# Kernel optimization log

Measured on AMD Instinct MI355X. Metric: run time of the kernel, lower is better.

Reference implementation:

```python
import jax, jax.numpy as jnp
import numpy as np

TOPK = 12
D = 256
SCALE = D ** -0.5


def setup_inputs() -> dict:
    key = jax.random.key(0)
    ks = jax.random.split(key, 6)
    N, D_in = 12288, 1024
    def w(k, shape, fan_in):
        return jax.random.normal(k, shape, jnp.float32) / np.float32(np.sqrt(fan_in))
    return {
        "x_path": jax.random.normal(ks[0], (N, D_in), jnp.float32),
        "wsi_w": w(ks[1], (D_in, D), D_in),
        "wsi_b": jnp.zeros((D,), jnp.float32),
        "wh_w": w(ks[2], (D, D), D),
        "wh_b": jnp.zeros((D,), jnp.float32),
        "wt_w": w(ks[3], (D, D), D),
        "wt_b": jnp.zeros((D,), jnp.float32),
        "w1_w": w(ks[4], (D, D), D),
        "w1_b": jnp.zeros((D,), jnp.float32),
        "w2_w": w(ks[5], (D, D), D),
        "w2_b": jnp.zeros((D,), jnp.float32),
    }


def reference(x_path, wsi_w, wsi_b, wh_w, wh_b, wt_w, wt_b, w1_w, w1_b, w2_w, w2_b):
    # wsi_net: Linear(1024,256) + ReLU (dropout is identity in eval)
    h = jax.nn.relu(x_path @ wsi_w + wsi_b)          # [N, D]
    e_h = h @ wh_w + wh_b                            # [N, D]
    e_t = h @ wt_w + wt_b                            # [N, D]
    # dense scaled similarity: [N, N]
    attn_logit = (e_h * SCALE) @ e_t.T
    topk_weight, topk_index = jax.lax.top_k(attn_logit, TOPK)  # [N, K]
    topk_prob = jax.nn.softmax(topk_weight, axis=-1)           # [N, K]
    # gather top-k neighbor tail embeddings
    Nb_h = e_t[topk_index]                           # [N, K, D]
    # eh_r = p * Nb_h + (1-p) (x) e_h   (outer product == broadcast mul)
    eh_r = topk_prob[..., None] * Nb_h + (1.0 - topk_prob)[..., None] * e_h[:, None, :]
    gate = jnp.tanh(e_h[:, None, :] + eh_r)          # [N, K, D]
    ka_weight = jnp.einsum('nkd,nkd->nk', Nb_h, gate)  # [N, K]
    ka_prob = jax.nn.softmax(ka_weight, axis=-1)       # [N, K]
    e_Nh = jnp.einsum('nk,nkd->nd', ka_prob, Nb_h)     # [N, D]
    sum_embedding = jax.nn.relu((e_h + e_Nh) @ w1_w + w1_b)
    bi_embedding = jax.nn.relu((e_h * e_Nh) @ w2_w + w2_b)
    return sum_embedding + bi_embedding              # [N, D]
```

## Files before the change

kernel.cpp:

```cpp
#include <hip/hip_runtime.h>
#include <hip/hip_bf16.h>
#include <cmath>

#define TK 12
#define NROW 12288
#define NEG_BIG (-3.0e38f)
#define MFMA16(a,b,c) __builtin_amdgcn_mfma_f32_16x16x32_f16(a,b,c,0,0,0)

#define NCH 8
#define CTILES 96
#define NPH 48
#define NGRP_TOT 384
#define CAP 256

typedef _Float16 f16x8 __attribute__((ext_vector_type(8)));
typedef _Float16 f16x4 __attribute__((ext_vector_type(4)));
typedef float    f32x4 __attribute__((ext_vector_type(4)));

typedef __attribute__((address_space(1))) const void gvoid_t;
typedef __attribute__((address_space(3))) void lvoid_t;
__device__ __forceinline__ void gload_lds16(const void* g, void* l) {
    __builtin_amdgcn_global_load_lds((gvoid_t*)g, (lvoid_t*)l, 16, 0, 0);
}

__global__ __launch_bounds__(256) void wpack(
    const float* __restrict__ W, _Float16* __restrict__ hi,
    _Float16* __restrict__ lo, int N, int nkt)
{
    const int tid = blockIdx.x * 256 + threadIdx.x;
    const int l = tid & 63;
    const int s = (tid >> 6) % nkt;
    const int cg = tid / (nkt * 64);
    const int krow = s * 32 + 8 * (l >> 4);
    const int col = cg * 16 + (l & 15);
    f16x8 H, L;
    #pragma unroll
    for (int j = 0; j < 8; ++j) {
        float w = W[(size_t)(krow + j) * N + col];
        _Float16 h = (_Float16)w;
        H[j] = h;
        L[j] = (_Float16)(w - (float)h);
    }
    *(f16x8*)(hi + (size_t)tid * 8) = H;
    *(f16x8*)(lo + (size_t)tid * 8) = L;
}

__global__ __launch_bounds__(256) void wpack4(
    const float* __restrict__ W0, const float* __restrict__ W1,
    const float* __restrict__ W2, const float* __restrict__ W3,
    _Float16* __restrict__ base)
{
    const int m = blockIdx.y;
    const float* W = (m == 0) ? W0 : (m == 1) ? W1 : (m == 2) ? W2 : W3;
    _Float16* hi = base + (size_t)m * 131072;
    _Float16* lo = hi + 65536;
    const int tid = blockIdx.x * 256 + threadIdx.x;
    const int l = tid & 63;
    const int s = (tid >> 6) & 7;
    const int cg = tid >> 9;
    const int krow = s * 32 + 8 * (l >> 4);
    const int col = cg * 16 + (l & 15);
    f16x8 H, L;
    #pragma unroll
    for (int j = 0; j < 8; ++j) {
        float w = W[(size_t)(krow + j) * 256 + col];
        _Float16 h = (_Float16)w;
        H[j] = h;
        L[j] = (_Float16)(w - (float)h);
    }
    *(f16x8*)(hi + (size_t)tid * 8) = H;
    *(f16x8*)(lo + (size_t)tid * 8) = L;
}

template<bool RELU>
__global__ __launch_bounds__(256) void gemm_mfma(
    const float* __restrict__ A1,
    const _Float16* __restrict__ Wh, const _Float16* __restrict__ Wl,
    const float* __restrict__ bias, float* __restrict__ C, int K)
{
    __shared__ _Float16 aH[2048], aL[2048];
    __shared__ _Float16 wH[2048], wL[2048];
    const int tid = threadIdx.x, lane = tid & 63, wave = tid >> 6;
    const int rb = blockIdx.y * 64;
    const int cbg = blockIdx.x * 4;
    const int nkt = K >> 5;

    const int arow = rb + wave * 16 + (lane & 15);
    const int acol0 = 8 * (lane >> 4);
    const float* a1p = A1 + (size_t)arow * K + acol0;
    const size_t wbase = ((size_t)(cbg + wave) * nkt) * 512 + lane * 8;

    f32x4 acc[4];
    #pragma unroll
    for (int rg = 0; rg < 4; ++rg) acc[rg] = (f32x4){0.f,0.f,0.f,0.f};

    float4 pa0 = *(const float4*)(a1p);
    float4 pa1 = *(const float4*)(a1p + 4);
    f16x8 pwh = *(const f16x8*)(Wh + wbase);
    f16x8 pwl = *(const f16x8*)(Wl + wbase);

    for (int kt = 0; kt < nkt; ++kt) {
        __syncthreads();
        {
            float v[8] = {pa0.x, pa0.y, pa0.z, pa0.w, pa1.x, pa1.y, pa1.z, pa1.w};
            f16x8 H, L;
            #pragma unroll
            for (int j = 0; j < 8; ++j) {
                _Float16 h = (_Float16)v[j];
                H[j] = h;
                L[j] = (_Float16)(v[j] - (float)h);
            }
            *(f16x8*)&aH[tid*8] = H;
            *(f16x8*)&aL[tid*8] = L;
            *(f16x8*)&wH[tid*8] = pwh;
            *(f16x8*)&wL[tid*8] = pwl;
        }
        __syncthreads();
        if (kt + 1 < nkt) {
            pa0 = *(const float4*)(a1p + (kt+1)*32);
            pa1 = *(const float4*)(a1p + (kt+1)*32 + 4);
            pwh = *(const f16x8*)(Wh + wbase + (size_t)(kt+1)*512);
            pwl = *(const f16x8*)(Wl + wbase + (size_t)(kt+1)*512);
        }
        f16x8 wh = *(const f16x8*)&wH[(wave*64 + lane)*8];
        f16x8 wl = *(const f16x8*)&wL[(wave*64 + lane)*8];
        #pragma unroll
        for (int rg = 0; rg < 4; ++rg) {
            f16x8 ah = *(const f16x8*)&aH[(rg*64 + lane)*8];
            f16x8 al = *(const f16x8*)&aL[(rg*64 + lane)*8];
            acc[rg] = MFMA16(wh, ah, acc[rg]);
            acc[rg] = MFMA16(wl, ah, acc[rg]);
            acc[rg] = MFMA16(wh, al, acc[rg]);
        }
    }
    const int col = (cbg + wave)*16 + 4*(lane >> 4);
    float4 b4 = *(const float4*)(bias + col);
    #pragma unroll
    for (int rg = 0; rg < 4; ++rg) {
        const int row = rb + rg*16 + (lane & 15);
        float4 o;
        o.x = acc[rg][0] + b4.x; o.y = acc[rg][1] + b4.y;
        o.z = acc[rg][2] + b4.z; o.w = acc[rg][3] + b4.w;
        if (RELU) {
            o.x = fmaxf(o.x, 0.f); o.y = fmaxf(o.y, 0.f);
            o.z = fmaxf(o.z, 0.f); o.w = fmaxf(o.w, 0.f);
        }
        *(float4*)(C + (size_t)row*256 + col) = o;
    }
}

template<int DMODE>
__global__ __launch_bounds__(256) void gemm_dual(
    const float* __restrict__ A1, const float* __restrict__ A2,
    const _Float16* __restrict__ W1h, const _Float16* __restrict__ W1l,
    const _Float16* __restrict__ W2h, const _Float16* __restrict__ W2l,
    const float* __restrict__ bias1, const float* __restrict__ bias2,
    float* __restrict__ C1, float* __restrict__ C2,
    _Float16* __restrict__ P1, _Float16* __restrict__ P2)
{
    __shared__ _Float16 aH[2][2048], aL[2][2048];
    __shared__ _Float16 wH[2][2048], wL[2][2048];
    const int tid = threadIdx.x, lane = tid & 63, wave = tid >> 6;
    const int rb = blockIdx.y * 64;
    const int cbg = blockIdx.x * 4;

    const int arow = rb + wave * 16 + (lane & 15);
    const int acol0 = 8 * (lane >> 4);
    const float* a1p = A1 + (size_t)arow * 256 + acol0;
    const float* a2p = (DMODE == 1) ? (A2 + (size_t)arow * 256 + acol0) : nullptr;
    const size_t wbase = ((size_t)(cbg + wave) * 8) * 512 + lane * 8;

    f32x4 acc1[4], acc2[4];
    #pragma unroll
    for (int rg = 0; rg < 4; ++rg) {
        acc1[rg] = (f32x4){0.f,0.f,0.f,0.f};
        acc2[rg] = (f32x4){0.f,0.f,0.f,0.f};
    }

    float4 pa0 = *(const float4*)(a1p);
    float4 pa1 = *(const float4*)(a1p + 4);
    float4 pb0, pb1;
    if (DMODE == 1) { pb0 = *(const float4*)(a2p); pb1 = *(const float4*)(a2p + 4); }
    f16x8 pw1h = *(const f16x8*)(W1h + wbase);
    f16x8 pw1l = *(const f16x8*)(W1l + wbase);
    f16x8 pw2h = *(const f16x8*)(W2h + wbase);
    f16x8 pw2l = *(const f16x8*)(W2l + wbase);

    for (int kt = 0; kt < 8; ++kt) {
        __syncthreads();
        {
            float v[8] = {pa0.x, pa0.y, pa0.z, pa0.w, pa1.x, pa1.y, pa1.z, pa1.w};
            if (DMODE == 0) {
                f16x8 H, L;
                #pragma unroll
                for (int j = 0; j < 8; ++j) {
                    _Float16 h = (_Float16)v[j];
                    H[j] = h;
                    L[j] = (_Float16)(v[j] - (float)h);
                }
                *(f16x8*)&aH[0][tid*8] = H;
                *(f16x8*)&aL[0][tid*8] = L;
            } else {
                float b[8] = {pb0.x, pb0.y, pb0.z, pb0.w, pb1.x, pb1.y, pb1.z, pb1.w};
                f16x8 Hs, Ls, Hm, Lm;
                #pragma unroll
                for (int j = 0; j < 8; ++j) {
                    float s = v[j] + b[j];
                    float m = v[j] * b[j];
                    _Float16 hs = (_Float16)s;
                    _Float16 hm = (_Float16)m;
                    Hs[j] = hs; Ls[j] = (_Float16)(s - (float)hs);
                    Hm[j] = hm; Lm[j] = (_Float16)(m - (float)hm);
                }
                *(f16x8*)&aH[0][tid*8] = Hs;
                *(f16x8*)&aL[0][tid*8] = Ls;
                *(f16x8*)&aH[1][tid*8] = Hm;
                *(f16x8*)&aL[1][tid*8] = Lm;
            }
            *(f16x8*)&wH[0][tid*8] = pw1h;
            *(f16x8*)&wL[0][tid*8] = pw1l;
            *(f16x8*)&wH[1][tid*8] = pw2h;
            *(f16x8*)&wL[1][tid*8] = pw2l;
        }
        __syncthreads();
        if (kt + 1 < 8) {
            pa0 = *(const float4*)(a1p + (kt+1)*32);
            pa1 = *(const float4*)(a1p + (kt+1)*32 + 4);
            if (DMODE == 1) {
                pb0 = *(const float4*)(a2p + (kt+1)*32);
                pb1 = *(const float4*)(a2p + (kt+1)*32 + 4);
            }
            pw1h = *(const f16x8*)(W1h + wbase + (size_t)(kt+1)*512);
            pw1l = *(const f16x8*)(W1l + wbase + (size_t)(kt+1)*512);
            pw2h = *(const f16x8*)(W2h + wbase + (size_t)(kt+1)*512);
            pw2l = *(const f16x8*)(W2l + wbase + (size_t)(kt+1)*512);
        }
        f16x8 w1h = *(const f16x8*)&wH[0][(wave*64 + lane)*8];
        f16x8 w1l = *(const f16x8*)&wL[0][(wave*64 + lane)*8];
        f16x8 w2h = *(const f16x8*)&wH[1][(wave*64 + lane)*8];
        f16x8 w2l = *(const f16x8*)&wL[1][(wave*64 + lane)*8];
        #pragma unroll
        for (int rg = 0; rg < 4; ++rg) {
            f16x8 ah0 = *(const f16x8*)&aH[0][(rg*64 + lane)*8];
            f16x8 al0 = *(const f16x8*)&aL[0][(rg*64 + lane)*8];
            acc1[rg] = MFMA16(w1h, ah0, acc1[rg]);
            acc1[rg] = MFMA16(w1l, ah0, acc1[rg]);
            acc1[rg] = MFMA16(w1h, al0, acc1[rg]);
            f16x8 ah1 = (DMODE == 1) ? *(const f16x8*)&aH[1][(rg*64 + lane)*8] : ah0;
            f16x8 al1 = (DMODE == 1) ? *(const f16x8*)&aL[1][(rg*64 + lane)*8] : al0;
            acc2[rg] = MFMA16(w2h, ah1, acc2[rg]);
            acc2[rg] = MFMA16(w2l, ah1, acc2[rg]);
            acc2[rg] = MFMA16(w2h, al1, acc2[rg]);
        }
    }
    const int col = (cbg + wave)*16 + 4*(lane >> 4);
    float4 b14 = *(const float4*)(bias1 + col);
    float4 b24 = *(const float4*)(bias2 + col);
    #pragma unroll
    for (int rg = 0; rg < 4; ++rg) {
        const int row = rb + rg*16 + (lane & 15);
        if (DMODE == 0) {
            float4 o1, o2;
            o1.x = acc1[rg][0] + b14.x; o1.y = acc1[rg][1] + b14.y;
            o1.z = acc1[rg][2] + b14.z; o1.w = acc1[rg][3] + b14.w;
            o2.x = acc2[rg][0] + b24.x; o2.y = acc2[rg][1] + b24.y;
            o2.z = acc2[rg][2] + b24.z; o2.w = acc2[rg][3] + b24.w;
            *(float4*)(C1 + (size_t)row*256 + col) = o1;
            *(float4*)(C2 + (size_t)row*256 + col) = o2;
            const size_t poff = ((size_t)(row >> 4)*8 + (col >> 5))*512
                              + (((col & 31) >> 3)*16 + (row & 15))*8 + (col & 7);
            f16x4 p1, p2;
            p1[0] = (_Float16)(o1.x * 0.0625f); p1[1] = (_Float16)(o1.y * 0.0625f);
            p1[2] = (_Float16)(o1.z * 0.0625f); p1[3] = (_Float16)(o1.w * 0.0625f);
            p2[0] = (_Float16)o2.x; p2[1] = (_Float16)o2.y;
            p2[2] = (_Float16)o2.z; p2[3] = (_Float16)o2.w;
            *(f16x4*)(P1 + poff) = p1;
            *(f16x4*)(P2 + poff) = p2;
        } else {
            float4 o;
            o.x = fmaxf(acc1[rg][0] + b14.x, 0.f) + fmaxf(acc2[rg][0] + b24.x, 0.f);
            o.y = fmaxf(acc1[rg][1] + b14.y, 0.f) + fmaxf(acc2[rg][1] + b24.y, 0.f);
            o.z = fmaxf(acc1[rg][2] + b14.z, 0.f) + fmaxf(acc2[rg][2] + b24.z, 0.f);
            o.w = fmaxf(acc1[rg][3] + b14.w, 0.f) + fmaxf(acc2[rg][3] + b24.w, 0.f);
            *(float4*)(C1 + (size_t)row*256 + col) = o;
        }
    }
}

__global__ __launch_bounds__(256, 2) void s1_gmax(
    const _Float16* __restrict__ ehh, const _Float16* __restrict__ eth,
    unsigned* __restrict__ g32, unsigned char* __restrict__ gcol)
{
    __shared__ _Float16 abuf[3][8192];
    const int tid = threadIdx.x, lane = tid & 63, wave = tid >> 6;
    const int chunk = blockIdx.x & (NCH-1);
    const int rblk = blockIdx.x >> 3;
    const int rg0 = rblk * 8 + wave * 2;

    f16x8 bh[2][8];
    #pragma unroll
    for (int rs = 0; rs < 2; ++rs) {
        const _Float16* p = ehh + (size_t)(rg0 + rs)*4096 + lane*8;
        #pragma unroll
        for (int s = 0; s < 8; ++s) bh[rs][s] = *(const f16x8*)(p + s*512);
    }
    #pragma unroll
    for (int rs = 0; rs < 2; ++rs)
        #pragma unroll
        for (int s = 0; s < 8; ++s)
            asm volatile("" : "+v"(bh[rs][s]));

    const int rsw = (lane >> 4) & 1;
    const int myrow = (rg0 + rsw)*16 + (lane & 15);
    const size_t rowbase = (size_t)myrow*NGRP_TOT + chunk*NPH;

    const _Float16* gsrc = eth + (size_t)chunk * CTILES * 4096;
    #pragma unroll
    for (int ph = 0; ph < 2; ++ph) {
        #pragma unroll
        for (int i = 0; i < 4; ++i) {
            const int u = wave*4 + i;
            gload_lds16(gsrc + (size_t)(ph*2 + (u>>3))*4096 + (u&7)*512 + lane*8,
                        &abuf[ph][u*512]);
        }
    }
    asm volatile("s_waitcnt vmcnt(4) lgkmcnt(0)" ::: "memory");
    __builtin_amdgcn_s_barrier();
    asm volatile("" ::: "memory");

    int cur = 0;
    for (int pp = 0; pp < 6; ++pp) {
        unsigned resv[8];
        unsigned long long colv = 0;
        #pragma unroll
        for (int q = 0; q < 8; ++q) {
            const int p = pp*8 + q;
            int nx = cur + 2; if (nx >= 3) nx -= 3;
            if (p + 2 < NPH) {
                #pragma unroll
                for (int i = 0; i < 4; ++i) {
                    const int u = wave*4 + i;
                    gload_lds16(gsrc + (size_t)((p+2)*2 + (u>>3))*4096 + (u&7)*512 + lane*8,
                                &abuf[nx][u*512]);
                }
            }
            float m1a = NEG_BIG, m2a = NEG_BIG; int mca = 0;
            float m1b = NEG_BIG, m2b = NEG_BIG; int mcb = 0;
            __builtin_amdgcn_s_setprio(1);
            #pragma unroll
            for (int tt = 0; tt < 2; ++tt) {
                f32x4 aE[2], aO[2];
                #pragma unroll
                for (int rs = 0; rs < 2; ++rs) {
                    aE[rs] = (f32x4){0.f,0.f,0.f,0.f};
                    aO[rs] = (f32x4){0.f,0.f,0.f,0.f};
                }
                #pragma unroll
                for (int s = 0; s < 8; ++s) {
                    f16x8 ah = *(const f16x8*)&abuf[cur][tt*4096 + s*512 + lane*8];
                    if (s & 1) {
                        aO[0] = MFMA16(ah, bh[0][s], aO[0]);
                        aO[1] = MFMA16(ah, bh[1][s], aO[1]);
                    } else {
                        aE[0] = MFMA16(ah, bh[0][s], aE[0]);
                        aE[1] = MFMA16(ah, bh[1][s], aE[1]);
                    }
                }
                f32x4 a0 = aE[0] + aO[0];
                f32x4 a1 = aE[1] + aO[1];
                const int cb = tt*16 + 4*(lane >> 4);
                #pragma unroll
                for (int e = 0; e < 4; ++e) {
                    bool g0 = a0[e] > m1a;
                    m2a = fmaxf(m2a, g0 ? m1a : a0[e]);
                    mca = g0 ? (cb + e) : mca;
                    m1a = fmaxf(m1a, a0[e]);
                    bool g1 = a1[e] > m1b;
                    m2b = fmaxf(m2b, g1 ? m1b : a1[e]);
                    mcb = g1 ? (cb + e) : mcb;
                    m1b = fmaxf(m1b, a1[e]);
                }
            }
            __builtin_amdgcn_s_setprio(0);
            #pragma unroll
            for (int k = 16; k <= 32; k <<= 1) {
                float o1 = __shfl_xor(m1a, k); int oc = __shfl_xor(mca, k);
                float o2 = __shfl_xor(m2a, k);
                bool gt = o1 > m1a;
                m2a = fmaxf(fmaxf(m2a, o2), gt ? m1a : o1);
                mca = gt ? oc : mca;
                m1a = fmaxf(m1a, o1);
                float p1 = __shfl_xor(m1b, k); int pc = __shfl_xor(mcb, k);
                float p2 = __shfl_xor(m2b, k);
                bool ht = p1 > m1b;
                m2b = fmaxf(fmaxf(m2b, p2), ht ? m1b : p1);
                mcb = ht ? pc : mcb;
                m1b = fmaxf(m1b, p1);
            }
            {
                float M1 = rsw ? m1b : m1a;
                float M2 = rsw ? m2b : m2a;
                int   MC = rsw ? mcb : mca;
                unsigned short h1 = __builtin_bit_cast(unsigned short, (_Float16)M1);
                unsigned short h2 = __builtin_bit_cast(unsigned short, (_Float16)M2);
                resv[q] = ((unsigned)h1 << 16) | h2;
                colv |= (unsigned long long)(unsigned char)MC << (8*q);
            }
            if (q == 7 && lane < 32) {
                const size_t base = rowbase + pp*8;
                uint4 v0; v0.x = resv[0]; v0.y = resv[1]; v0.z = resv[2]; v0.w = resv[3];
                uint4 v1; v1.x = resv[4]; v1.y = resv[5]; v1.z = resv[6]; v1.w = resv[7];
                *(uint4*)(g32 + base)     = v0;
                *(uint4*)(g32 + base + 4) = v1;
                *(unsigned long long*)(gcol + base) = colv;
            }
            if (p + 2 < NPH) {
                if (q == 7) { asm volatile("s_waitcnt vmcnt(7)" ::: "memory"); }
                else        { asm volatile("s_waitcnt vmcnt(4)" ::: "memory"); }
            } else {
                asm volatile("s_waitcnt vmcnt(0)" ::: "memory");
            }
            __builtin_amdgcn_s_barrier();
            asm volatile("" ::: "memory");
            cur = cur + 1; if (cur >= 3) cur = 0;
        }
    }
    asm volatile("s_waitcnt vmcnt(0)" ::: "memory");
}

__global__ __launch_bounds__(256) void b2s3(
    const unsigned* __restrict__ g32, const unsigned char* __restrict__ gcol,
    const float* __restrict__ e_h, const float* __restrict__ e_t,
    float* __restrict__ e_Nh)
{
    __shared__ int cbuf[4][CAP];
    const int lane = threadIdx.x & 63;
    const int wave = threadIdx.x >> 6;
    const int row  = blockIdx.x * 4 + wave;

    const unsigned* gr = g32 + (size_t)row*NGRP_TOT + lane*6;
    uint2 u0 = *(const uint2*)gr;
    uint2 u1 = *(const uint2*)(gr + 2);
    uint2 u2 = *(const uint2*)(gr + 4);
    unsigned uu[6] = {u0.x, u0.y, u1.x, u1.y, u2.x, u2.y};
    float m1[6], m2[6];
    #pragma unroll
    for (int i = 0; i < 6; ++i) {
        m1[i] = (float)__builtin_bit_cast(_Float16, (unsigned short)(uu[i] >> 16));
        m2[i] = (float)__builtin_bit_cast(_Float16, (unsigned short)(uu[i] & 0xffffu));
    }
    float sl[6];
    #pragma unroll
    for (int j = 0; j < 6; ++j) sl[j] = NEG_BIG;
    #pragma unroll
    for (int i = 0; i < 6; ++i) {
        float vv = m1[i];
        #pragma unroll
        for (int j = 5; j >= 1; --j)
            sl[j] = __builtin_amdgcn_fmed3f(vv, sl[j], sl[j-1]);
        sl[0] = fmaxf(vv, sl[0]);
    }
    int hi = 0;
    float t12 = NEG_BIG;
    #pragma unroll 1
    for (int o = 0; o < TK; ++o) {
        float head = (hi < 6) ? sl[hi] : NEG_BIG;
        float bv = head; int bl = lane;
        #pragma unroll
        for (int off = 1; off <= 32; off <<= 1) {
            float ov = __shfl_xor(bv, off);
            int   ol = __shfl_xor(bl, off);
            bool take = (ov > bv) || (ov == bv && ol < bl);
            bv = take ? ov : bv;
            bl = take ? ol : bl;
        }
        if (lane == bl) hi++;
        t12 = bv;
    }
    const float tau = t12 - 0.02f;

    int n = 0;
    int* crow = cbuf[wave];
    #pragma unroll 1
    for (int i = 0; i < 6; ++i) {
        const bool hit1 = m1[i] >= tau;
        const bool expn = hit1 && (m2[i] >= tau);
        const bool single = hit1 && !expn;
        unsigned long long ms = __ballot(single);
        if (single) {
            const int pos = n + __popcll(ms & ((1ull << lane) - 1ull));
            if (pos < CAP) {
                const int g = lane*6 + i;
                crow[pos] = g*32 + (int)gcol[(size_t)row*NGRP_TOT + g];
            }
        }
        n += __popcll(ms);
        unsigned long long me = __ballot(expn);
        while (me) {
            const int src = __builtin_ctzll(me);
            me &= me - 1ull;
            const int cb = (src*6 + i) * 32;
            if (lane < 32) {
                const int pos = n + lane;
                if (pos < CAP) crow[pos] = cb + lane;
            }
            n += 32;
        }
    }
    const int cn = (n < CAP) ? n : CAP;

    const float* ehr = e_h + (size_t)row * 256;
    float v[4]; int c[4];
    #pragma unroll
    for (int i = 0; i < 4; ++i) {
        const int idx = lane + 64*i;
        const bool act = idx < cn;
        c[i] = act ? crow[idx] : (0x7ffffff0 + i);
        v[i] = NEG_BIG;
        if (cn > 64*i) {
            const float* etr = e_t + (size_t)(act ? c[i] : 0) * 256;
            float s = 0.f;
            for (int k = 0; k < 64; ++k) {
                float4 a = *(const float4*)(ehr + k*4);
                float4 b = *(const float4*)(etr + k*4);
                s += a.x*b.x + a.y*b.y + a.z*b.z + a.w*b.w;
            }
            if (act) v[i] = s * 0.0625f;
        }
    }

    float tvv[TK]; int ti[TK];
    #pragma unroll
    for (int o = 0; o < TK; ++o) {
        float bv = v[0]; int bc = c[0];
        #pragma unroll
        for (int i = 1; i < 4; ++i) {
            bool take = (v[i] > bv) || (v[i] == bv && c[i] < bc);
            bv = take ? v[i] : bv;
            bc = take ? c[i] : bc;
        }
        #pragma unroll
        for (int off = 32; off; off >>= 1) {
            float ov = __shfl_xor(bv, off);
            int   oc = __shfl_xor(bc, off);
            bool take = (ov > bv) || (ov == bv && oc < bc);
            bv = take ? ov : bv;
            bc = take ? oc : bc;
        }
        tvv[o] = bv; ti[o] = bc;
        #pragma unroll
        for (int i = 0; i < 4; ++i)
            if (c[i] == bc) v[i] = NEG_BIG;
    }

    float p[TK]; float Z = 0.f;
    #pragma unroll
    for (int j = 0; j < TK; ++j) { p[j] = expf(tvv[j] - tvv[0]); Z += p[j]; }
    const float invZ = 1.f / Z;
    #pragma unroll
    for (int j = 0; j < TK; ++j) p[j] *= invZ;

    float4 eh = *(const float4*)(ehr + lane * 4);

    float4 nb[TK]; float kw[TK];
    #pragma unroll
    for (int k = 0; k < TK; ++k) {
        float4 nn = *(const float4*)(e_t + (size_t)ti[k] * 256 + lane * 4);
        nb[k] = nn;
        const float pk = p[k], qk = 1.f - p[k];
        float4 gt;
        gt.x = tanhf(eh.x + (pk * nn.x + qk * eh.x));
        gt.y = tanhf(eh.y + (pk * nn.y + qk * eh.y));
        gt.z = tanhf(eh.z + (pk * nn.z + qk * eh.z));
        gt.w = tanhf(eh.w + (pk * nn.w + qk * eh.w));
        float d = nn.x*gt.x + nn.y*gt.y + nn.z*gt.z + nn.w*gt.w;
        #pragma unroll
        for (int off = 32; off; off >>= 1) d += __shfl_xor(d, off);
        kw[k] = d;
    }

    float km = kw[0];
    #pragma unroll
    for (int k = 1; k < TK; ++k) km = fmaxf(km, kw[k]);
    float kz = 0.f; float kp[TK];
    #pragma unroll
    for (int k = 0; k < TK; ++k) { kp[k] = expf(kw[k] - km); kz += kp[k]; }
    const float invKZ = 1.f / kz;

    float4 acc = make_float4(0.f, 0.f, 0.f, 0.f);
    #pragma unroll
    for (int k = 0; k < TK; ++k) {
        acc.x += kp[k] * nb[k].x;
        acc.y += kp[k] * nb[k].y;
        acc.z += kp[k] * nb[k].z;
        acc.w += kp[k] * nb[k].w;
    }
    acc.x *= invKZ; acc.y *= invKZ; acc.z *= invKZ; acc.w *= invKZ;
    *(float4*)(e_Nh + (size_t)row * 256 + lane * 4) = acc;
}

extern "C" void kernel_launch(void* const* d_in, const int* in_sizes, int n_in,
                              void* d_out, int out_size, void* d_ws, size_t ws_size,
                              hipStream_t stream)
{
    (void)in_sizes; (void)n_in; (void)out_size; (void)ws_size;
    const float* x     = (const float*)d_in[0];
    const float* wsi_w = (const float*)d_in[1];
    const float* wsi_b = (const float*)d_in[2];
    const float* wh_w  = (const float*)d_in[3];
    const float* wh_b  = (const float*)d_in[4];
    const float* wt_w  = (const float*)d_in[5];
    const float* wt_b  = (const float*)d_in[6];
    const float* w1_w  = (const float*)d_in[7];
    const float* w1_b  = (const float*)d_in[8];
    const float* w2_w  = (const float*)d_in[9];
    const float* w2_b  = (const float*)d_in[10];
    float* out = (float*)d_out;
    float* ws  = (float*)d_ws;

    const int M = NROW;
    const size_t ND = (size_t)M * 256;

    float* h    = ws;
    float* e_h  = ws + ND;
    float* e_t  = ws + 2*ND;
    _Float16* ehh = (_Float16*)(ws + 3*ND);
    _Float16* eth = (_Float16*)(ws + 3*ND + ND/2);
    size_t o = 4*ND;
    unsigned* g32 = (unsigned*)(ws + o);          o += (size_t)NGRP_TOT*NROW;
    unsigned char* gcol = (unsigned char*)(ws + o); o += (size_t)NGRP_TOT*NROW/4;
    _Float16* hp = (_Float16*)(ws + o);
    _Float16* wsiH = hp;
    _Float16* wsiL = hp + 262144;
    _Float16* w4base = hp + 524288;
    _Float16* whH  = w4base;
    _Float16* whL  = w4base + 65536;
    _Float16* wtH  = w4base + 2*65536;
    _Float16* wtL  = w4base + 3*65536;
    _Float16* w1H  = w4base + 4*65536;
    _Float16* w1L  = w4base + 5*65536;
    _Float16* w2H  = w4base + 6*65536;
    _Float16* w2L  = w4base + 7*65536;
    float* e_Nh = h;

    wpack<<<128, 256, 0, stream>>>(wsi_w, wsiH, wsiL, 256, 32);
    wpack4<<<dim3(32, 4), 256, 0, stream>>>(wh_w, wt_w, w1_w, w2_w, w4base);

    gemm_mfma<true><<<dim3(4, M/64), 256, 0, stream>>>(
        x, wsiH, wsiL, wsi_b, h, 1024);
    gemm_dual<0><<<dim3(4, M/64), 256, 0, stream>>>(
        h, nullptr, whH, whL, wtH, wtL, wh_b, wt_b, e_h, e_t, ehh, eth);
    s1_gmax<<<NCH*96, 256, 0, stream>>>(ehh, eth, g32, gcol);
    b2s3<<<M/4, 256, 0, stream>>>(g32, gcol, e_h, e_t, e_Nh);
    gemm_dual<1><<<dim3(4, M/64), 256, 0, stream>>>(
        e_h, e_Nh, w1H, w1L, w2H, w2L, w1_b, w2_b, out, nullptr, nullptr, nullptr);
}
```

Before: 336.4 us.

## Merge weight-pack kernels, use fast exp/tanh/divide, drop setprio in similarity loop

Combines the two weight packing kernels into one launch, saving one launch. Replaces tanhf/expf/division in the gather-softmax stage with fast intrinsic versions built on __expf and __fdividef, which lowers ALU cost but can slightly reduce accuracy. It also removes the s_setprio hints around the MFMA block in the similarity kernel, which may change how waves are scheduled relative to the loads.

```diff
diff --git a/kernel.cpp b/kernel.cpp
--- a/kernel.cpp
+++ b/kernel.cpp
@@ -23,53 +23,58 @@
     __builtin_amdgcn_global_load_lds((gvoid_t*)g, (lvoid_t*)l, 16, 0, 0);
 }
 
-__global__ __launch_bounds__(256) void wpack(
-    const float* __restrict__ W, _Float16* __restrict__ hi,
-    _Float16* __restrict__ lo, int N, int nkt)
-{
-    const int tid = blockIdx.x * 256 + threadIdx.x;
-    const int l = tid & 63;
-    const int s = (tid >> 6) % nkt;
-    const int cg = tid / (nkt * 64);
-    const int krow = s * 32 + 8 * (l >> 4);
-    const int col = cg * 16 + (l & 15);
-    f16x8 H, L;
-    #pragma unroll
-    for (int j = 0; j < 8; ++j) {
-        float w = W[(size_t)(krow + j) * N + col];
-        _Float16 h = (_Float16)w;
-        H[j] = h;
-        L[j] = (_Float16)(w - (float)h);
-    }
-    *(f16x8*)(hi + (size_t)tid * 8) = H;
-    *(f16x8*)(lo + (size_t)tid * 8) = L;
-}
-
-__global__ __launch_bounds__(256) void wpack4(
+__device__ __forceinline__ float ftanh(float x) {
+    float e = __expf(2.f * x);
+    return 1.f - __fdividef(2.f, e + 1.f);
+}
+
+__global__ __launch_bounds__(256) void wpack_all(
+    const float* __restrict__ Wsi, _Float16* __restrict__ wsiH,
+    _Float16* __restrict__ wsiL,
     const float* __restrict__ W0, const float* __restrict__ W1,
     const float* __restrict__ W2, const float* __restrict__ W3,
     _Float16* __restrict__ base)
 {
-    const int m = blockIdx.y;
-    const float* W = (m == 0) ? W0 : (m == 1) ? W1 : (m == 2) ? W2 : W3;
-    _Float16* hi = base + (size_t)m * 131072;
-    _Float16* lo = hi + 65536;
-    const int tid = blockIdx.x * 256 + threadIdx.x;
-    const int l = tid & 63;
-    const int s = (tid >> 6) & 7;
-    const int cg = tid >> 9;
-    const int krow = s * 32 + 8 * (l >> 4);
-    const int col = cg * 16 + (l & 15);
-    f16x8 H, L;
-    #pragma unroll
-    for (int j = 0; j < 8; ++j) {
-        float w = W[(size_t)(krow + j) * 256 + col];
-        _Float16 h = (_Float16)w;
-        H[j] = h;
-        L[j] = (_Float16)(w - (float)h);
-    }
-    *(f16x8*)(hi + (size_t)tid * 8) = H;
-    *(f16x8*)(lo + (size_t)tid * 8) = L;
+    const int bx = blockIdx.x;
+    if (bx < 128) {
+        const int tid = bx * 256 + threadIdx.x;
+        const int l = tid & 63;
+        const int s = (tid >> 6) & 31;
+        const int cg = tid >> 11;
+        const int krow = s * 32 + 8 * (l >> 4);
+        const int col = cg * 16 + (l & 15);
+        f16x8 H, L;
+        #pragma unroll
+        for (int j = 0; j < 8; ++j) {
+            float w = Wsi[(size_t)(krow + j) * 256 + col];
+            _Float16 h = (_Float16)w;
+            H[j] = h;
+            L[j] = (_Float16)(w - (float)h);
+        }
+        *(f16x8*)(wsiH + (size_t)tid * 8) = H;
+        *(f16x8*)(wsiL + (size_t)tid * 8) = L;
+    } else {
+        const int m = (bx - 128) >> 5;
+        const float* W = (m == 0) ? W0 : (m == 1) ? W1 : (m == 2) ? W2 : W3;
+        _Float16* hi = base + (size_t)m * 131072;
+        _Float16* lo = hi + 65536;
+        const int tid = ((bx - 128) & 31) * 256 + threadIdx.x;
+        const int l = tid & 63;
+        const int s = (tid >> 6) & 7;
+        const int cg = tid >> 9;
+        const int krow = s * 32 + 8 * (l >> 4);
+        const int col = cg * 16 + (l & 15);
+        f16x8 H, L;
+        #pragma unroll
+        for (int j = 0; j < 8; ++j) {
+            float w = W[(size_t)(krow + j) * 256 + col];
+            _Float16 h = (_Float16)w;
+            H[j] = h;
+            L[j] = (_Float16)(w - (float)h);
+        }
+        *(f16x8*)(hi + (size_t)tid * 8) = H;
+        *(f16x8*)(lo + (size_t)tid * 8) = L;
+    }
 }
 
 template<bool RELU>
@@ -346,7 +351,6 @@
             }
             float m1a = NEG_BIG, m2a = NEG_BIG; int mca = 0;
             float m1b = NEG_BIG, m2b = NEG_BIG; int mcb = 0;
-            __builtin_amdgcn_s_setprio(1);
             #pragma unroll
             for (int tt = 0; tt < 2; ++tt) {
                 f32x4 aE[2], aO[2];
@@ -381,7 +385,6 @@
                     m1b = fmaxf(m1b, a1[e]);
                 }
             }
-            __builtin_amdgcn_s_setprio(0);
             #pragma unroll
             for (int k = 16; k <= 32; k <<= 1) {
                 float o1 = __shfl_xor(m1a, k); int oc = __shfl_xor(mca, k);
@@ -555,8 +558,8 @@
 
     float p[TK]; float Z = 0.f;
     #pragma unroll
-    for (int j = 0; j < TK; ++j) { p[j] = expf(tvv[j] - tvv[0]); Z += p[j]; }
-    const float invZ = 1.f / Z;
+    for (int j = 0; j < TK; ++j) { p[j] = __expf(tvv[j] - tvv[0]); Z += p[j]; }
+    const float invZ = __fdividef(1.f, Z);
     #pragma unroll
     for (int j = 0; j < TK; ++j) p[j] *= invZ;
 
@@ -569,10 +572,10 @@
         nb[k] = nn;
         const float pk = p[k], qk = 1.f - p[k];
         float4 gt;
-        gt.x = tanhf(eh.x + (pk * nn.x + qk * eh.x));
-        gt.y = tanhf(eh.y + (pk * nn.y + qk * eh.y));
-        gt.z = tanhf(eh.z + (pk * nn.z + qk * eh.z));
-        gt.w = tanhf(eh.w + (pk * nn.w + qk * eh.w));
+        gt.x = ftanh(eh.x + (pk * nn.x + qk * eh.x));
+        gt.y = ftanh(eh.y + (pk * nn.y + qk * eh.y));
+        gt.z = ftanh(eh.z + (pk * nn.z + qk * eh.z));
+        gt.w = ftanh(eh.w + (pk * nn.w + qk * eh.w));
         float d = nn.x*gt.x + nn.y*gt.y + nn.z*gt.z + nn.w*gt.w;
         #pragma unroll
         for (int off = 32; off; off >>= 1) d += __shfl_xor(d, off);
@@ -584,8 +587,8 @@
     for (int k = 1; k < TK; ++k) km = fmaxf(km, kw[k]);
     float kz = 0.f; float kp[TK];
     #pragma unroll
-    for (int k = 0; k < TK; ++k) { kp[k] = expf(kw[k] - km); kz += kp[k]; }
-    const float invKZ = 1.f / kz;
+    for (int k = 0; k < TK; ++k) { kp[k] = __expf(kw[k] - km); kz += kp[k]; }
+    const float invKZ = __fdividef(1.f, kz);
 
     float4 acc = make_float4(0.f, 0.f, 0.f, 0.f);
     #pragma unroll
@@ -643,8 +646,8 @@
     _Float16* w2L  = w4base + 7*65536;
     float* e_Nh = h;
 
-    wpack<<<128, 256, 0, stream>>>(wsi_w, wsiH, wsiL, 256, 32);
-    wpack4<<<dim3(32, 4), 256, 0, stream>>>(wh_w, wt_w, w1_w, w2_w, w4base);
+    wpack_all<<<256, 256, 0, stream>>>(wsi_w, wsiH, wsiL,
+                                       wh_w, wt_w, w1_w, w2_w, w4base);
 
     gemm_mfma<true><<<dim3(4, M/64), 256, 0, stream>>>(
         x, wsiH, wsiL, wsi_b, h, 1024);
```

Result: faster. 319.0 us (-5.1%).
